# Kernel optimization log

Hardware: AMD Instinct MI355X
Metric: run time of the kernel (lower is better)

Reference implementation:

```python
import jax, jax.numpy as jnp
import numpy as np

B, L, DIM, S, K = 8, 4096, 512, 32, 8
THR = 0.5
EPS = 1e-8


def clin(z, Wr, Wi):
    # complex linear on [..., d_in, 2] -> [..., d_out, 2]
    zr, zi = z[..., 0], z[..., 1]
    return jnp.stack([zr @ Wr - zi @ Wi, zr @ Wi + zi @ Wr], axis=-1)


def setup_inputs() -> dict:
    key = jax.random.key(0)
    ks = jax.random.split(key, 8)
    s = DIM ** -0.5
    return {
        "z": jax.random.normal(ks[0], (B, L, DIM, 2), jnp.float32),
        "slot_keys": jnp.zeros((B, S, DIM, 2), jnp.float32),
        "slot_values": jnp.zeros((B, S, DIM, 2), jnp.float32),
        "slot_mask": jnp.zeros((B, S), jnp.float32),
        "W_sal_r": jax.random.normal(ks[1], (DIM, 1), jnp.float32) * s,
        "W_sal_i": jax.random.normal(ks[2], (DIM, 1), jnp.float32) * s,
        "score_bias": jnp.full((1,), -1.0, jnp.float32),
        "novelty_scale": jnp.ones((1,), jnp.float32),
        "W_ek_r": jax.random.normal(ks[3], (DIM, DIM), jnp.float32) * s,
        "W_ek_i": jax.random.normal(ks[4], (DIM, DIM), jnp.float32) * s,
        "W_ev_r": jax.random.normal(ks[5], (DIM, DIM), jnp.float32) * s,
        "W_ev_i": jax.random.normal(ks[6], (DIM, DIM), jnp.float32) * s,
        "W_rq_r": jax.random.normal(ks[7], (DIM, DIM), jnp.float32) * s,
        "W_rq_i": jax.random.normal(jax.random.fold_in(key, 99), (DIM, DIM), jnp.float32) * s,
        "norm_gain": jnp.ones((DIM,), jnp.float32),
    }


def _forward(z, slot_keys, slot_values, slot_mask, W_sal_r, W_sal_i, score_bias,
             novelty_scale, W_ek_r, W_ek_i, W_ev_r, W_ev_i, W_rq_r, W_rq_i, norm_gain):
    b, l, dim, _ = z.shape
    # --- EventSalienceHead ---
    proj = clin(z, W_sal_r, W_sal_i)                 # [B,L,1,2]
    phase = jnp.sqrt(proj[..., 0] ** 2 + proj[..., 1] ** 2 + EPS)[..., 0]  # [B,L]
    mag = jnp.sqrt(z[..., 0] ** 2 + z[..., 1] ** 2 + EPS)                  # [B,L,dim]
    avg_mag = mag.mean(-1)                            # [B,L]
    pad = jnp.pad(avg_mag, ((0, 0), (2, 2)))         # avg_pool1d k=5, count_include_pad
    local_mean = sum(pad[:, i:i + l] for i in range(5)) / 5.0
    novelty = (avg_mag - local_mean) * novelty_scale[0]
    salience = jax.nn.sigmoid(phase + novelty + score_bias[0])  # [B,L]

    # --- vectorized span detection (cumsum boundary trick) ---
    above = salience > THR                            # [B,L]
    prev = jnp.pad(above[:, :-1], ((0, 0), (1, 0)))   # shifted right, False at t=0
    start = above & ~prev                             # span starts
    ev_idx = jnp.cumsum(start.astype(jnp.int32), axis=1) - 1  # 0-based span index
    valid = above & (ev_idx >= 0) & (ev_idx < S)      # spans beyond S are dropped
    b_idx = jnp.arange(b, dtype=jnp.int32)[:, None]
    seg = jnp.where(valid, b_idx * S + ev_idx, b * S).reshape(-1)   # [B*L]
    sal_w = jnp.where(valid, salience, 0.0).reshape(-1)             # [B*L]

    # --- salience-weighted span pooling via segment_sum ---
    num = jax.ops.segment_sum(sal_w[:, None, None] * z.reshape(-1, dim, 2),
                              seg, num_segments=b * S + 1)[: b * S]
    den = jax.ops.segment_sum(sal_w, seg, num_segments=b * S + 1)[: b * S]
    event_vecs = (num / jnp.maximum(den, EPS)[:, None, None]).reshape(b, S, dim, 2)
    event_mask = (den > 0).astype(z.dtype).reshape(b, S)            # [B,S]

    # --- slot write (ptr=0, n_write=S -> slot i gets event i if valid) ---
    event_keys = clin(event_vecs, W_ek_r, W_ek_i)
    event_values = clin(event_vecs, W_ev_r, W_ev_i)
    m = event_mask[:, :, None, None]
    new_keys = m * event_keys + (1.0 - m) * slot_keys
    new_values = m * event_values + (1.0 - m) * slot_values
    new_mask = jnp.minimum(slot_mask + event_mask, 1.0)

    # --- phase-coherence read (cosine scores, top-k) ---
    queries = clin(z, W_rq_r, W_rq_i)
    qr, qi = queries[..., 0], queries[..., 1]
    kr, ki = new_keys[..., 0], new_keys[..., 1]
    dot = jnp.einsum('bld,bsd->bls', qr, kr) + jnp.einsum('bld,bsd->bls', qi, ki)
    q_mag = jnp.sqrt((qr ** 2 + qi ** 2).sum(-1, keepdims=True) + EPS)     # [B,L,1]
    k_mag = jnp.sqrt((kr ** 2 + ki ** 2).sum(-1) + EPS)[:, None, :]        # [B,1,S]
    scores = dot / (q_mag * k_mag + EPS)
    scores = jnp.where(new_mask[:, None, :] == 0, -1e9, scores)
    top_s, top_i = jax.lax.top_k(scores, K)            # [B,L,K]
    attn = jax.nn.softmax(top_s, axis=-1)
    # scatter top-k attn back to [B,L,S] then one bmm (avoids [B,L,K,dim,2] gather)
    bi = jnp.arange(b)[:, None, None]
    li = jnp.arange(l)[None, :, None]
    attn_full = jnp.zeros((b, l, S), scores.dtype).at[bi, li, top_i].add(attn)
    vr = jnp.einsum('bls,bsd->bld', attn_full, new_values[..., 0])
    vi = jnp.einsum('bls,bsd->bld', attn_full, new_values[..., 1])
    retrieved = jnp.stack([vr, vi], axis=-1)           # [B,L,dim,2]

    # --- ComplexNorm: RMS over per-element complex magnitude, learned gain ---
    rms = jnp.sqrt((retrieved[..., 0] ** 2 + retrieved[..., 1] ** 2).mean(-1, keepdims=True) + EPS)
    out = retrieved / rms[..., None] * norm_gain[None, None, :, None]
    return out, new_keys, new_values, new_mask, salience


def reference(z, slot_keys, slot_values, slot_mask, W_sal_r, W_sal_i, score_bias,
              novelty_scale, W_ek_r, W_ek_i, W_ev_r, W_ev_i, W_rq_r, W_rq_i, norm_gain):
    return _forward(z, slot_keys, slot_values, slot_mask, W_sal_r, W_sal_i, score_bias,
                    novelty_scale, W_ek_r, W_ek_i, W_ev_r, W_ev_i, W_rq_r, W_rq_i, norm_gain)
```

## Files before the change

### kernel.cpp

```cpp
#include <hip/hip_runtime.h>
#include <math.h>

#define NB 8
#define NL 4096
#define NDIM 512
#define NS 32
#define NTOP 8
#define FEPS 1e-8f
#define NM (NB*NL)

typedef unsigned short u16;
typedef unsigned int u32;
typedef __attribute__((ext_vector_type(8))) __bf16 bf16x8;
typedef __attribute__((ext_vector_type(4))) float f32x4;

__device__ __forceinline__ u16 f2bf_rne(float f) {
  u32 u = __float_as_uint(f);
  u32 r = (u + 0x7fffu + ((u >> 16) & 1u)) >> 16;
  return (u16)r;
}

__device__ __forceinline__ void gload16(const u16* g, u16* l) {
  __builtin_amdgcn_global_load_lds(
      (const __attribute__((address_space(1))) u32*)(g),
      (__attribute__((address_space(3))) u32*)(l), 16, 0, 0);
}

__global__ __launch_bounds__(256) void k_phase(
    const float4* __restrict__ z4, const float2* __restrict__ wr2,
    const float2* __restrict__ wi2, float* __restrict__ phase,
    float* __restrict__ avgmag, u16* __restrict__ A) {
  int lane = threadIdx.x & 63;
  int m = blockIdx.x * 4 + (threadIdx.x >> 6);
  const float4* row = z4 + (size_t)m * 256;
  u16* arow = A + (size_t)m * 1024;
  float pr = 0.f, pi = 0.f, ms = 0.f;
#pragma unroll
  for (int j = 0; j < 4; j++) {
    int idx = lane + 64 * j;
    float4 v = row[idx];
    float2 wr = wr2[idx], wi = wi2[idx];
    pr += v.x * wr.x - v.y * wi.x + v.z * wr.y - v.w * wi.y;
    pi += v.x * wi.x + v.y * wr.x + v.z * wi.y + v.w * wr.y;
    ms += sqrtf(v.x * v.x + v.y * v.y + FEPS) + sqrtf(v.z * v.z + v.w * v.w + FEPS);
    u32 zr_pk = ((u32)f2bf_rne(v.z) << 16) | (u32)f2bf_rne(v.x);
    u32 zi_pk = ((u32)f2bf_rne(v.w) << 16) | (u32)f2bf_rne(v.y);
    *(u32*)&arow[2 * idx] = zr_pk;
    *(u32*)&arow[512 + 2 * idx] = zi_pk;
  }
#pragma unroll
  for (int off = 32; off >= 1; off >>= 1) {
    pr += __shfl_xor(pr, off);
    pi += __shfl_xor(pi, off);
    ms += __shfl_xor(ms, off);
  }
  if (lane == 0) {
    phase[m] = sqrtf(pr * pr + pi * pi + FEPS);
    avgmag[m] = ms * (1.0f / 512.0f);
  }
}

__global__ __launch_bounds__(256) void k_scan(
    const float* __restrict__ phase, const float* __restrict__ avgmag,
    const float* __restrict__ bias_p, const float* __restrict__ ns_p,
    float* __restrict__ salO, int* __restrict__ estart, int* __restrict__ eend) {
  __shared__ float am[NL];
  __shared__ int abv[NL];
  __shared__ int cnt[256];
  int b = blockIdx.x, t = threadIdx.x;
  size_t gb = (size_t)b * NL;
  if (t < NS) { estart[b * NS + t] = -1; eend[b * NS + t] = -1; }
  for (int i = t; i < NL; i += 256) am[i] = avgmag[gb + i];
  __syncthreads();
  float bias = bias_p[0], ns = ns_p[0];
  for (int i = t; i < NL; i += 256) {
    float lm = am[i];
    if (i >= 2) lm += am[i - 2];
    if (i >= 1) lm += am[i - 1];
    if (i <= NL - 2) lm += am[i + 1];
    if (i <= NL - 3) lm += am[i + 2];
    lm *= 0.2f;
    float x = phase[gb + i] + (am[i] - lm) * ns + bias;
    float s = 1.0f / (1.0f + expf(-x));
    salO[gb + i] = s;
    abv[i] = (s > 0.5f) ? 1 : 0;
  }
  __syncthreads();
  int c = 0, l0 = t * 16;
  for (int j = 0; j < 16; j++) {
    int l = l0 + j;
    int a = abv[l];
    int p = (l == 0) ? 0 : abv[l - 1];
    c += (a && !p) ? 1 : 0;
  }
  cnt[t] = c;
  __syncthreads();
  for (int off = 1; off < 256; off <<= 1) {
    int v = (t >= off) ? cnt[t - off] : 0;
    __syncthreads();
    cnt[t] += v;
    __syncthreads();
  }
  c = (t > 0) ? cnt[t - 1] : 0;
  for (int j = 0; j < 16; j++) {
    int l = l0 + j;
    int a = abv[l];
    int p = (l == 0) ? 0 : abv[l - 1];
    int st = (a && !p) ? 1 : 0;
    c += st;
    int ev = c - 1;
    if (a && ev >= 0 && ev < NS) {
      if (st) estart[b * NS + ev] = l;
      int nxt = (l == NL - 1) ? 0 : abv[l + 1];
      if (!nxt) eend[b * NS + ev] = l + 1;
    }
  }
}

__global__ __launch_bounds__(256) void k_event(
    const float4* __restrict__ z4, const float* __restrict__ salO,
    const int* __restrict__ estart, const int* __restrict__ eend,
    float4* __restrict__ evec4, float* __restrict__ emask) {
  int i = blockIdx.x;
  int b = i >> 5;
  int t = threadIdx.x;
  int st = estart[i];
  int en = (st >= 0) ? eend[i] : 0;
  if (st < 0) st = 0;
  float4 acc = {0.f, 0.f, 0.f, 0.f};
  float den = 0.f;
  for (int l = st; l < en; l++) {
    float w = salO[(size_t)b * NL + l];
    float4 v = z4[((size_t)b * NL + l) * 256 + t];
    acc.x += w * v.x; acc.y += w * v.y; acc.z += w * v.z; acc.w += w * v.w;
    den += w;
  }
  float inv = 1.0f / fmaxf(den, FEPS);
  float4 o = {acc.x * inv, acc.y * inv, acc.z * inv, acc.w * inv};
  evec4[(size_t)i * 256 + t] = o;
  if (t == 0) emask[i] = (den > 0.f) ? 1.0f : 0.0f;
}

__global__ __launch_bounds__(256) void k_kv(
    const float* __restrict__ evec, const float* __restrict__ emask,
    const float* __restrict__ Wekr, const float* __restrict__ Weki,
    const float* __restrict__ Wevr, const float* __restrict__ Wevi,
    const float* __restrict__ slotK, const float* __restrict__ slotV,
    const float* __restrict__ slotM, float* __restrict__ newK,
    float* __restrict__ newV, float* __restrict__ newM,
    float* __restrict__ kmag) {
  __shared__ float ev[1024];
  __shared__ float red[256];
  int i = blockIdx.x, t = threadIdx.x;
  for (int j = t; j < 1024; j += 256) ev[j] = evec[(size_t)i * 1024 + j];
  __syncthreads();
  int d0 = t, d1 = t + 256;
  float kr0 = 0, ki0 = 0, kr1 = 0, ki1 = 0;
  float vr0 = 0, vi0 = 0, vr1 = 0, vi1 = 0;
  for (int k = 0; k < NDIM; k++) {
    float er = ev[2 * k], ei = ev[2 * k + 1];
    int o = k * NDIM;
    float a0 = Wekr[o + d0], a1 = Wekr[o + d1];
    float b0 = Weki[o + d0], b1 = Weki[o + d1];
    kr0 += er * a0 - ei * b0; ki0 += er * b0 + ei * a0;
    kr1 += er * a1 - ei * b1; ki1 += er * b1 + ei * a1;
    a0 = Wevr[o + d0]; a1 = Wevr[o + d1];
    b0 = Wevi[o + d0]; b1 = Wevi[o + d1];
    vr0 += er * a0 - ei * b0; vi0 += er * b0 + ei * a0;
    vr1 += er * a1 - ei * b1; vi1 += er * b1 + ei * a1;
  }
  float m = emask[i];
  const float2* sk = (const float2*)slotK + (size_t)i * NDIM;
  const float2* sv = (const float2*)slotV + (size_t)i * NDIM;
  float2 s0 = sk[d0], s1 = sk[d1], t0 = sv[d0], t1 = sv[d1];
  float nkr0 = (m > 0.f) ? kr0 : s0.x, nki0 = (m > 0.f) ? ki0 : s0.y;
  float nkr1 = (m > 0.f) ? kr1 : s1.x, nki1 = (m > 0.f) ? ki1 : s1.y;
  float nvr0 = (m > 0.f) ? vr0 : t0.x, nvi0 = (m > 0.f) ? vi0 : t0.y;
  float nvr1 = (m > 0.f) ? vr1 : t1.x, nvi1 = (m > 0.f) ? vi1 : t1.y;
  float2* nk = (float2*)newK + (size_t)i * NDIM;
  float2* nv = (float2*)newV + (size_t)i * NDIM;
  nk[d0] = {nkr0, nki0}; nk[d1] = {nkr1, nki1};
  nv[d0] = {nvr0, nvi0}; nv[d1] = {nvr1, nvi1};
  red[t] = nkr0 * nkr0 + nki0 * nki0 + nkr1 * nkr1 + nki1 * nki1;
  __syncthreads();
  for (int off = 128; off >= 1; off >>= 1) {
    if (t < off) red[t] += red[t + off];
    __syncthreads();
  }
  if (t == 0) {
    kmag[i] = sqrtf(red[0] + FEPS);
    newM[i] = fminf(slotM[i] + m, 1.0f);
  }
}

__global__ __launch_bounds__(256) void k_wbf16(
    const float* __restrict__ Wr, const float* __restrict__ Wi,
    u16* __restrict__ BT) {
  __shared__ float tile[64][65];
  int bx = blockIdx.x & 15;
  int by = blockIdx.x >> 4;
  int k0 = bx * 64, n0 = by * 64;
  int t = threadIdx.x;
  int c = t & 63, r0 = t >> 6;
  const float* src;
  float sgn = 1.f;
  int kk0 = k0 & 511, nn0 = n0 & 511;
  if (k0 < 512) {
    src = (n0 < 512) ? Wr : Wi;
  } else {
    if (n0 < 512) { src = Wi; sgn = -1.f; }
    else          { src = Wr; }
  }
  for (int j = r0; j < 64; j += 4)
    tile[j][c] = sgn * src[(size_t)(kk0 + j) * 512 + nn0 + c];
  __syncthreads();
  for (int j = r0; j < 64; j += 4) {
    float v = tile[c][j];
    BT[(size_t)(n0 + j) * 1024 + k0 + c] = f2bf_rne(v);
  }
}

__global__ __launch_bounds__(256) void k_qmag(
    const u16* __restrict__ A, const u16* __restrict__ BT,
    float* __restrict__ qpart) {
  __shared__ __align__(16) u16 As[128 * 32];
  __shared__ __align__(16) u16 Bs[128 * 32];
  int bid = blockIdx.x;
  int work = (bid & 7) * 256 + (bid >> 3);
  int mt = work >> 3, nt = work & 7;
  int m0 = mt * 128, n0 = nt * 128;
  int t = threadIdx.x;
  int lane = t & 63, w = t >> 6;
  int wr = w >> 1, wc = w & 1;
  int lrow = lane & 15, kg = lane >> 4;
  int grow = w * 16 + (lane >> 2);
  int gcol = (lane & 3) * 8;
  const u16* gA = A  + (size_t)(m0 + grow) * 1024 + gcol;
  const u16* gB = BT + (size_t)(n0 + grow) * 1024 + gcol;
  u16* lA = As + w * 512;
  u16* lB = Bs + w * 512;

  f32x4 acc[4][4];
#pragma unroll
  for (int i = 0; i < 4; i++)
#pragma unroll
    for (int j = 0; j < 4; j++)
#pragma unroll
      for (int r = 0; r < 4; r++) acc[i][j][r] = 0.f;

  for (int kt = 0; kt < 1024; kt += 32) {
    gload16(gA + kt, lA);
    gload16(gA + 64 * 1024 + kt, lA + 2048);
    gload16(gB + kt, lB);
    gload16(gB + 64 * 1024 + kt, lB + 2048);
    __syncthreads();
    bf16x8 af[4], bfr[4];
#pragma unroll
    for (int i = 0; i < 4; i++)
      af[i] = *(const bf16x8*)&As[(wr * 64 + i * 16 + lrow) * 32 + kg * 8];
#pragma unroll
    for (int j = 0; j < 4; j++)
      bfr[j] = *(const bf16x8*)&Bs[(wc * 64 + j * 16 + lrow) * 32 + kg * 8];
#pragma unroll
    for (int i = 0; i < 4; i++)
#pragma unroll
      for (int j = 0; j < 4; j++)
        acc[i][j] = __builtin_amdgcn_mfma_f32_16x16x32_bf16(af[i], bfr[j], acc[i][j], 0, 0, 0);
    __syncthreads();
  }
#pragma unroll
  for (int i = 0; i < 4; i++)
#pragma unroll
    for (int r = 0; r < 4; r++) {
      float s = 0.f;
#pragma unroll
      for (int j = 0; j < 4; j++) { float v = acc[i][j][r]; s += v * v; }
      s += __shfl_xor(s, 1); s += __shfl_xor(s, 2);
      s += __shfl_xor(s, 4); s += __shfl_xor(s, 8);
      if (lrow == 0)
        qpart[(size_t)(m0 + wr * 64 + i * 16 + kg * 4 + r) * 16 + nt * 2 + wc] = s;
    }
}

__global__ __launch_bounds__(256) void k_gvec(
    const float* __restrict__ newK, const float* __restrict__ Wr,
    const float* __restrict__ Wi, float* __restrict__ g) {
  __shared__ float kr[512], ki[512];
  int blk = blockIdx.x;
  int i = blk >> 1, h = blk & 1;
  int t = threadIdx.x;
  const float2* krow = (const float2*)newK + (size_t)i * 512;
  for (int j = t; j < 512; j += 256) { float2 v = krow[j]; kr[j] = v.x; ki[j] = v.y; }
  __syncthreads();
  int j = t + h * 256;
  float glo = 0, ghi = 0;
  const float4* wr0 = (const float4*)(Wr + (size_t)j * 512);
  const float4* wi0 = (const float4*)(Wi + (size_t)j * 512);
  const float4* kr4 = (const float4*)kr;
  const float4* ki4 = (const float4*)ki;
  for (int n4 = 0; n4 < 128; n4++) {
    float4 a = wr0[n4], b = wi0[n4];
    float4 kk = kr4[n4], qq = ki4[n4];
    glo += a.x * kk.x + b.x * qq.x + a.y * kk.y + b.y * qq.y
         + a.z * kk.z + b.z * qq.z + a.w * kk.w + b.w * qq.w;
    ghi += a.x * qq.x - b.x * kk.x + a.y * qq.y - b.y * kk.y
         + a.z * qq.z - b.z * kk.z + a.w * qq.w - b.w * kk.w;
  }
  float* go = g + (size_t)i * 1024;
  go[j] = glo;
  go[512 + j] = ghi;
}

__global__ __launch_bounds__(256) void k_dot(
    const float4* __restrict__ z4, const float* __restrict__ g,
    float* __restrict__ dotb) {
  __shared__ float gs[16 * 1024];
  int blk = blockIdx.x;
  int b = blk >> 6, chunk = blk & 63;
  int t = threadIdx.x, lane = t & 63, w = t >> 6;
  int mbase = b * 4096 + chunk * 64 + w * 16;
  for (int p = 0; p < 2; p++) {
    __syncthreads();
    {
      const float4* gsrc = (const float4*)(g + (size_t)b * 32768 + p * 16384);
      float4* gd = (float4*)gs;
      for (int j = t; j < 4096; j += 256) gd[j] = gsrc[j];
    }
    __syncthreads();
    for (int it = 0; it < 4; it++) {
      int m = mbase + it * 4;
      float4 zr0[4], zr1[4], zr2[4], zr3[4];
#pragma unroll
      for (int jj = 0; jj < 4; jj++) {
        zr0[jj] = z4[(size_t)(m + 0) * 256 + lane + 64 * jj];
        zr1[jj] = z4[(size_t)(m + 1) * 256 + lane + 64 * jj];
        zr2[jj] = z4[(size_t)(m + 2) * 256 + lane + 64 * jj];
        zr3[jj] = z4[(size_t)(m + 3) * 256 + lane + 64 * jj];
      }
      float myd0 = 0, myd1 = 0, myd2 = 0, myd3 = 0;
      for (int s = 0; s < 16; s++) {
        float p0 = 0, p1 = 0, p2 = 0, p3 = 0;
        const float2* gl = (const float2*)(gs + s * 1024);
#pragma unroll
        for (int jj = 0; jj < 4; jj++) {
          int idx = lane + 64 * jj;
          float2 lo = gl[idx], hi = gl[256 + idx];
          p0 += zr0[jj].x * lo.x + zr0[jj].z * lo.y + zr0[jj].y * hi.x + zr0[jj].w * hi.y;
          p1 += zr1[jj].x * lo.x + zr1[jj].z * lo.y + zr1[jj].y * hi.x + zr1[jj].w * hi.y;
          p2 += zr2[jj].x * lo.x + zr2[jj].z * lo.y + zr2[jj].y * hi.x + zr2[jj].w * hi.y;
          p3 += zr3[jj].x * lo.x + zr3[jj].z * lo.y + zr3[jj].y * hi.x + zr3[jj].w * hi.y;
        }
#pragma unroll
        for (int off = 32; off >= 1; off >>= 1) {
          p0 += __shfl_xor(p0, off);
          p1 += __shfl_xor(p1, off);
          p2 += __shfl_xor(p2, off);
          p3 += __shfl_xor(p3, off);
        }
        if (lane == s) { myd0 = p0; myd1 = p1; myd2 = p2; myd3 = p3; }
      }
      if (lane < 16) {
        int sidx = p * 16 + lane;
        dotb[(size_t)(m + 0) * 32 + sidx] = myd0;
        dotb[(size_t)(m + 1) * 32 + sidx] = myd1;
        dotb[(size_t)(m + 2) * 32 + sidx] = myd2;
        dotb[(size_t)(m + 3) * 32 + sidx] = myd3;
      }
    }
  }
}

__global__ __launch_bounds__(256) void k_attn2(
    const float* __restrict__ dotb, const float* __restrict__ qpart,
    const float* __restrict__ newV, const float* __restrict__ newM,
    const float* __restrict__ kmag, const float* __restrict__ gain,
    float* __restrict__ out0) {
  int lane = threadIdx.x & 63;
  int m = blockIdx.x * 4 + (threadIdx.x >> 6);
  int b = m >> 12;
  const float4* qp = (const float4*)(qpart + (size_t)m * 16);
  float4 q0 = qp[0], q1 = qp[1], q2 = qp[2], q3 = qp[3];
  float qs = q0.x + q0.y + q0.z + q0.w + q1.x + q1.y + q1.z + q1.w
           + q2.x + q2.y + q2.z + q2.w + q3.x + q3.y + q3.z + q3.w;
  float qmag = sqrtf(qs + FEPS);

  int s = lane & 31;
  float dot = dotb[(size_t)m * 32 + s];
  float km = kmag[b * NS + s];
  float sc = dot / (qmag * km + FEPS);
  if (newM[b * NS + s] == 0.0f) sc = -1.0e9f;
  float myscore = sc;

  float topv[NTOP];
  int topi[NTOP];
#pragma unroll
  for (int it = 0; it < NTOP; it++) {
    float val = myscore;
    int idx = lane & 31;
#pragma unroll
    for (int off = 32; off >= 1; off >>= 1) {
      float ov = __shfl_xor(val, off);
      int oi = __shfl_xor(idx, off);
      if (ov > val || (ov == val && oi < idx)) { val = ov; idx = oi; }
    }
    topv[it] = val;
    topi[it] = idx;
    if ((lane & 31) == idx) myscore = -3.0e38f;
  }
  float mx = topv[0];
  float w[NTOP], wsum = 0.f;
#pragma unroll
  for (int it = 0; it < NTOP; it++) { w[it] = expf(topv[it] - mx); wsum += w[it]; }
  float inv = 1.0f / wsum;

  const float2* V2p = (const float2*)newV + (size_t)b * NS * NDIM;
  float vr[8], vi[8];
#pragma unroll
  for (int j = 0; j < 8; j++) { vr[j] = 0.f; vi[j] = 0.f; }
#pragma unroll
  for (int it = 0; it < NTOP; it++) {
    float a = w[it] * inv;
    const float2* vrow = V2p + (size_t)topi[it] * NDIM;
#pragma unroll
    for (int j = 0; j < 8; j++) {
      float2 v = vrow[lane + 64 * j];
      vr[j] += a * v.x;
      vi[j] += a * v.y;
    }
  }
  float r2 = 0.f;
#pragma unroll
  for (int j = 0; j < 8; j++) r2 += vr[j] * vr[j] + vi[j] * vi[j];
#pragma unroll
  for (int off = 32; off >= 1; off >>= 1) r2 += __shfl_xor(r2, off);
  float rinv = 1.0f / sqrtf(r2 * (1.0f / 512.0f) + FEPS);

  float2* orow = (float2*)out0 + (size_t)m * NDIM;
#pragma unroll
  for (int j = 0; j < 8; j++) {
    int d = lane + 64 * j;
    float g = gain[d] * rinv;
    orow[d] = {vr[j] * g, vi[j] * g};
  }
}

extern "C" void kernel_launch(void* const* d_in, const int* in_sizes, int n_in,
                              void* d_out, int out_size, void* d_ws, size_t ws_size,
                              hipStream_t stream) {
  const float* z      = (const float*)d_in[0];
  const float* slotK  = (const float*)d_in[1];
  const float* slotV  = (const float*)d_in[2];
  const float* slotM  = (const float*)d_in[3];
  const float* Wsr    = (const float*)d_in[4];
  const float* Wsi    = (const float*)d_in[5];
  const float* sbias  = (const float*)d_in[6];
  const float* nscale = (const float*)d_in[7];
  const float* Wekr   = (const float*)d_in[8];
  const float* Weki   = (const float*)d_in[9];
  const float* Wevr   = (const float*)d_in[10];
  const float* Wevi   = (const float*)d_in[11];
  const float* Wrqr   = (const float*)d_in[12];
  const float* Wrqi   = (const float*)d_in[13];
  const float* gain   = (const float*)d_in[14];

  float* out = (float*)d_out;
  float* out0 = out;
  float* newK = out + 33554432;
  float* newV = newK + 262144;
  float* newM = newV + 262144;
  float* salO = newM + 256;

  float* ws = (float*)d_ws;
  float* phaseb = ws;
  float* avgmgb = phaseb + NM;
  float* evec   = avgmgb + NM;
  float* emask  = evec + 262144;
  float* kmagb  = emask + 256;
  float* gvec   = kmagb + 256;
  float* dotb   = gvec + 262144;
  float* qpart  = dotb + 1048576;
  int* estart   = (int*)(qpart + 524288);
  int* eend     = estart + 256;
  u16* BT       = (u16*)(eend + 256);
  u16* Abf      = BT + 1024 * 1024;

  k_wbf16<<<256, 256, 0, stream>>>(Wrqr, Wrqi, BT);
  k_phase<<<NM / 4, 256, 0, stream>>>((const float4*)z, (const float2*)Wsr,
                                      (const float2*)Wsi, phaseb, avgmgb, Abf);
  k_scan<<<NB, 256, 0, stream>>>(phaseb, avgmgb, sbias, nscale, salO, estart, eend);
  k_event<<<NB * NS, 256, 0, stream>>>((const float4*)z, salO, estart, eend,
                                       (float4*)evec, emask);
  k_kv<<<NB * NS, 256, 0, stream>>>(evec, emask, Wekr, Weki, Wevr, Wevi,
                                    slotK, slotV, slotM, newK, newV, newM, kmagb);
  k_qmag<<<2048, 256, 0, stream>>>(Abf, BT, qpart);
  k_gvec<<<NB * NS * 2, 256, 0, stream>>>(newK, Wrqr, Wrqi, gvec);
  k_dot<<<512, 256, 0, stream>>>((const float4*)z, gvec, dotb);
  k_attn2<<<NM / 4, 256, 0, stream>>>(dotb, qpart, newV, newM, kmagb, gain, out0);
}
```

Measured before the change: 772.1 us.

## Batch eight events per block in k_kv and move key magnitude into k_gvec

k_kv is restructured so each block processes 8 events against a 64-column slice of either the key or the value weight pair. Previously every event block streamed all four 512x512 weight matrices, so this cuts redundant weight reads and doubles the block count. The key-norm reduction is moved out of k_kv into k_gvec, which already loads each new key row. The cost is a smaller per-thread output tile and an extra reduction inside half of the k_gvec blocks.

```diff
diff --git a/kernel.cpp b/kernel.cpp
--- a/kernel.cpp
+++ b/kernel.cpp
@@ -147,50 +147,53 @@
     const float* __restrict__ Wevr, const float* __restrict__ Wevi,
     const float* __restrict__ slotK, const float* __restrict__ slotV,
     const float* __restrict__ slotM, float* __restrict__ newK,
-    float* __restrict__ newV, float* __restrict__ newM,
-    float* __restrict__ kmag) {
-  __shared__ float ev[1024];
-  __shared__ float red[256];
-  int i = blockIdx.x, t = threadIdx.x;
-  for (int j = t; j < 1024; j += 256) ev[j] = evec[(size_t)i * 1024 + j];
+    float* __restrict__ newV, float* __restrict__ newM) {
+  __shared__ float ev[8][1024];
+  __shared__ float em[8];
+  int blk = blockIdx.x;
+  int eg = blk >> 4;
+  int q  = blk & 15;
+  int matsel = q >> 3, dq = q & 7;
+  int i0 = eg * 8;
+  int t = threadIdx.x;
+  {
+    const float4* src = (const float4*)(evec + (size_t)i0 * 1024);
+    float4* dst = (float4*)&ev[0][0];
+    for (int j = t; j < 2048; j += 256) dst[j] = src[j];
+  }
+  if (t < 8) em[t] = emask[i0 + t];
   __syncthreads();
-  int d0 = t, d1 = t + 256;
-  float kr0 = 0, ki0 = 0, kr1 = 0, ki1 = 0;
-  float vr0 = 0, vi0 = 0, vr1 = 0, vi1 = 0;
-  for (int k = 0; k < NDIM; k++) {
-    float er = ev[2 * k], ei = ev[2 * k + 1];
-    int o = k * NDIM;
-    float a0 = Wekr[o + d0], a1 = Wekr[o + d1];
-    float b0 = Weki[o + d0], b1 = Weki[o + d1];
-    kr0 += er * a0 - ei * b0; ki0 += er * b0 + ei * a0;
-    kr1 += er * a1 - ei * b1; ki1 += er * b1 + ei * a1;
-    a0 = Wevr[o + d0]; a1 = Wevr[o + d1];
-    b0 = Wevi[o + d0]; b1 = Wevi[o + d1];
-    vr0 += er * a0 - ei * b0; vi0 += er * b0 + ei * a0;
-    vr1 += er * a1 - ei * b1; vi1 += er * b1 + ei * a1;
-  }
-  float m = emask[i];
-  const float2* sk = (const float2*)slotK + (size_t)i * NDIM;
-  const float2* sv = (const float2*)slotV + (size_t)i * NDIM;
-  float2 s0 = sk[d0], s1 = sk[d1], t0 = sv[d0], t1 = sv[d1];
-  float nkr0 = (m > 0.f) ? kr0 : s0.x, nki0 = (m > 0.f) ? ki0 : s0.y;
-  float nkr1 = (m > 0.f) ? kr1 : s1.x, nki1 = (m > 0.f) ? ki1 : s1.y;
-  float nvr0 = (m > 0.f) ? vr0 : t0.x, nvi0 = (m > 0.f) ? vi0 : t0.y;
-  float nvr1 = (m > 0.f) ? vr1 : t1.x, nvi1 = (m > 0.f) ? vi1 : t1.y;
-  float2* nk = (float2*)newK + (size_t)i * NDIM;
-  float2* nv = (float2*)newV + (size_t)i * NDIM;
-  nk[d0] = {nkr0, nki0}; nk[d1] = {nkr1, nki1};
-  nv[d0] = {nvr0, nvi0}; nv[d1] = {nvr1, nvi1};
-  red[t] = nkr0 * nkr0 + nki0 * nki0 + nkr1 * nkr1 + nki1 * nki1;
-  __syncthreads();
-  for (int off = 128; off >= 1; off >>= 1) {
-    if (t < off) red[t] += red[t + off];
-    __syncthreads();
-  }
-  if (t == 0) {
-    kmag[i] = sqrtf(red[0] + FEPS);
-    newM[i] = fminf(slotM[i] + m, 1.0f);
-  }
+  int dl = t & 63, eh = t >> 6;
+  int d = dq * 64 + dl;
+  int e0 = eh * 2, e1 = e0 + 1;
+  const float* Wr = matsel ? Wevr : Wekr;
+  const float* Wi = matsel ? Wevi : Weki;
+  const float* wrp = Wr + d;
+  const float* wip = Wi + d;
+  const float2* ep0 = (const float2*)ev[e0];
+  const float2* ep1 = (const float2*)ev[e1];
+  float ar0 = 0.f, ai0 = 0.f, ar1 = 0.f, ai1 = 0.f;
+#pragma unroll 8
+  for (int k = 0; k < 512; k++) {
+    float wr = wrp[(size_t)k * 512];
+    float wi = wip[(size_t)k * 512];
+    float2 x0 = ep0[k], x1 = ep1[k];
+    ar0 += x0.x * wr - x0.y * wi; ai0 += x0.x * wi + x0.y * wr;
+    ar1 += x1.x * wr - x1.y * wi; ai1 += x1.x * wi + x1.y * wr;
+  }
+  int ii0 = i0 + e0, ii1 = i0 + e1;
+  float m0 = em[e0], m1 = em[e1];
+  const float2* slot = (const float2*)(matsel ? slotV : slotK);
+  float2* outp = (float2*)(matsel ? newV : newK);
+  float2 sl0 = slot[(size_t)ii0 * NDIM + d];
+  float2 sl1 = slot[(size_t)ii1 * NDIM + d];
+  float2 o0, o1;
+  o0.x = (m0 > 0.f) ? ar0 : sl0.x; o0.y = (m0 > 0.f) ? ai0 : sl0.y;
+  o1.x = (m1 > 0.f) ? ar1 : sl1.x; o1.y = (m1 > 0.f) ? ai1 : sl1.y;
+  outp[(size_t)ii0 * NDIM + d] = o0;
+  outp[(size_t)ii1 * NDIM + d] = o1;
+  if (matsel == 0 && dq == 0 && t < 8)
+    newM[i0 + t] = fminf(slotM[i0 + t] + em[t], 1.0f);
 }
 
 __global__ __launch_bounds__(256) void k_wbf16(
@@ -284,14 +287,26 @@
 
 __global__ __launch_bounds__(256) void k_gvec(
     const float* __restrict__ newK, const float* __restrict__ Wr,
-    const float* __restrict__ Wi, float* __restrict__ g) {
+    const float* __restrict__ Wi, float* __restrict__ g,
+    float* __restrict__ kmag) {
   __shared__ float kr[512], ki[512];
+  __shared__ float red[256];
   int blk = blockIdx.x;
   int i = blk >> 1, h = blk & 1;
   int t = threadIdx.x;
   const float2* krow = (const float2*)newK + (size_t)i * 512;
   for (int j = t; j < 512; j += 256) { float2 v = krow[j]; kr[j] = v.x; ki[j] = v.y; }
   __syncthreads();
+  if (h == 0) {
+    red[t] = kr[t] * kr[t] + ki[t] * ki[t]
+           + kr[t + 256] * kr[t + 256] + ki[t + 256] * ki[t + 256];
+    __syncthreads();
+    for (int off = 128; off >= 1; off >>= 1) {
+      if (t < off) red[t] += red[t + off];
+      __syncthreads();
+    }
+    if (t == 0) kmag[i] = sqrtf(red[0] + FEPS);
+  }
   int j = t + h * 256;
   float glo = 0, ghi = 0;
   const float4* wr0 = (const float4*)(Wr + (size_t)j * 512);
@@ -490,10 +505,10 @@
   k_scan<<<NB, 256, 0, stream>>>(phaseb, avgmgb, sbias, nscale, salO, estart, eend);
   k_event<<<NB * NS, 256, 0, stream>>>((const float4*)z, salO, estart, eend,
                                        (float4*)evec, emask);
-  k_kv<<<NB * NS, 256, 0, stream>>>(evec, emask, Wekr, Weki, Wevr, Wevi,
-                                    slotK, slotV, slotM, newK, newV, newM, kmagb);
+  k_kv<<<512, 256, 0, stream>>>(evec, emask, Wekr, Weki, Wevr, Wevi,
+                                slotK, slotV, slotM, newK, newV, newM);
   k_qmag<<<2048, 256, 0, stream>>>(Abf, BT, qpart);
-  k_gvec<<<NB * NS * 2, 256, 0, stream>>>(newK, Wrqr, Wrqi, gvec);
+  k_gvec<<<NB * NS * 2, 256, 0, stream>>>(newK, Wrqr, Wrqi, gvec, kmagb);
   k_dot<<<512, 256, 0, stream>>>((const float4*)z, gvec, dotb);
   k_attn2<<<NM / 4, 256, 0, stream>>>(dotb, qpart, newV, newM, kmagb, gain, out0);
 }
```

New measurement: 671.9 us. -13.0%, faster.
